# Kernel optimization log

Hardware: AMD Instinct MI355X
Metric: run time of the kernel (lower is better)

The kernel has to match this reference:

```python
import jax, jax.numpy as jnp
import numpy as np

HEADS = 8
DIM_HEAD = 64
SCALE = DIM_HEAD ** -0.5
LN_EPS = 1e-5


def setup_inputs() -> dict:
    key = jax.random.key(0)
    ks = jax.random.split(key, 4)
    b, n, dim = 8, 1024, 512
    inner = HEADS * DIM_HEAD  # 512
    return {
        "x": jax.random.normal(ks[0], (b, n, dim), dtype=jnp.float32),
        "w_qkv": jax.random.normal(ks[1], (dim, 3 * inner), dtype=jnp.float32) * (dim ** -0.5),
        "reattn_w": jax.random.normal(ks[2], (HEADS, HEADS), dtype=jnp.float32),
        "ln_g": jnp.ones((HEADS,), dtype=jnp.float32),
        "ln_b": jnp.zeros((HEADS,), dtype=jnp.float32),
        "w_out": jax.random.normal(ks[3], (inner, dim), dtype=jnp.float32) * (inner ** -0.5),
        "b_out": jnp.zeros((dim,), dtype=jnp.float32),
    }


def reference(x, w_qkv, reattn_w, ln_g, ln_b, w_out, b_out):
    b, n, dim = x.shape
    h, d = HEADS, DIM_HEAD
    qkv = x @ w_qkv  # [b, n, 3*h*d]
    q, k, v = jnp.split(qkv, 3, axis=-1)
    to_heads = lambda t: t.reshape(b, n, h, d).transpose(0, 2, 1, 3)  # [b,h,n,d]
    q, k, v = to_heads(q), to_heads(k), to_heads(v)

    dots = jnp.einsum('bhid,bhjd->bhij', q, k) * SCALE
    attn = jax.nn.softmax(dots, axis=-1)  # dropout = 0 -> identity

    # cross-head re-mixing: b h i j, h g -> b g i j
    attn = jnp.einsum('bhij,hg->bgij', attn, reattn_w)

    # LayerNorm over the head dimension (axis=1 of [b,h,i,j])
    mu = jnp.mean(attn, axis=1, keepdims=True)
    var = jnp.var(attn, axis=1, keepdims=True)
    reattn = (attn - mu) * jax.lax.rsqrt(var + LN_EPS)
    reattn = reattn * ln_g[None, :, None, None] + ln_b[None, :, None, None]

    out = jnp.einsum('bhij,bhjd->bhid', reattn, v)
    out = out.transpose(0, 2, 1, 3).reshape(b, n, h * d)  # [b, n, inner]
    return out @ w_out + b_out
```

## Files before the change

kernel.cpp:

```cpp
#include <hip/hip_runtime.h>
#include <hip/hip_bf16.h>

typedef short bf16x8 __attribute__((ext_vector_type(8)));
typedef float f32x4 __attribute__((ext_vector_type(4)));

__device__ inline unsigned short f2bf(float f) {
    union { float f; unsigned u; } c; c.f = f;
    unsigned r = c.u + 0x7fffu + ((c.u >> 16) & 1u);
    return (unsigned short)(r >> 16);
}
__device__ inline float bf2f(unsigned short u) {
    union { unsigned u; float f; } c; c.u = ((unsigned)u) << 16; return c.f;
}
__device__ inline unsigned cvt_pk_bf16(float lo, float hi) {
    unsigned r;
    asm("v_cvt_pk_bf16_f32 %0, %1, %2" : "=v"(r) : "v"(lo), "v"(hi));
    return r;
}
__device__ inline float fast_exp2(float x) {
#if __has_builtin(__builtin_amdgcn_exp2f)
    return __builtin_amdgcn_exp2f(x);
#else
    return __exp2f(x);
#endif
}

__global__ __launch_bounds__(256) void k_f32_to_bf16(const float* __restrict__ in,
                                                     unsigned short* __restrict__ out, int n4) {
    int i = blockIdx.x * 256 + threadIdx.x;
    if (i >= n4) return;
    f32x4 v = *(const f32x4*)&in[(size_t)i * 4];
    ushort4 o;
    o.x = f2bf(v[0]); o.y = f2bf(v[1]); o.z = f2bf(v[2]); o.w = f2bf(v[3]);
    *(ushort4*)&out[(size_t)i * 4] = o;
}

__global__ __launch_bounds__(256) void k_transpose_bf16(const float* __restrict__ in,
                                                        unsigned short* __restrict__ out,
                                                        int K, int N) {
    int idx = blockIdx.x * 256 + threadIdx.x;
    if (idx >= N * K) return;
    int n = idx / K, k = idx % K;
    out[idx] = f2bf(in[(size_t)k * N + n]);
}

__global__ __launch_bounds__(256) void k_relayout(const unsigned short* __restrict__ qkv,
                                                  unsigned short* __restrict__ kt2,
                                                  unsigned short* __restrict__ vt2) {
    const int bh = blockIdx.y;
    const int b = bh >> 3, h = bh & 7;
    const int jt = blockIdx.x;
    const int t = threadIdx.x;
    __shared__ unsigned short tile[32][72];
    const int j = t >> 3, dc = (t & 7) * 8;
    const size_t qbase = (size_t)(b * 1024 + jt * 32 + j) * 1536;
    const size_t chunk = ((size_t)bh * 32 + jt) * 2048;
    bf16x8 kv = *(const bf16x8*)&qkv[qbase + 512 + h * 64 + dc];
    *(bf16x8*)&kt2[chunk + (dc >> 5) * 1024 + j * 32 + (dc & 31)] = kv;
    bf16x8 vv = *(const bf16x8*)&qkv[qbase + 1024 + h * 64 + dc];
    *(bf16x8*)&tile[j][dc] = vv;
    __syncthreads();
    const int d = t >> 2, j0 = (t & 3) * 8;
    union { bf16x8 v; unsigned short s[8]; } pk;
#pragma unroll
    for (int e = 0; e < 8; ++e) pk.s[e] = tile[j0 + e][d];
    *(bf16x8*)&vt2[chunk + d * 32 + j0] = pk.v;
}

template <int BM, int BN, int BK, bool OUT_BF16, bool HAS_BIAS>
__global__ __launch_bounds__(256) void gemm_bt(
    const unsigned short* __restrict__ A, int ldA, long long sA,
    const unsigned short* __restrict__ B, int ldB, long long sB,
    void* __restrict__ Cv, int ldC, long long sC,
    const float* __restrict__ bias, float scale, int K) {
    constexpr int PAD = 8, LDR = BK + PAD;
    __shared__ __align__(16) unsigned short As[BM * LDR];
    __shared__ __align__(16) unsigned short Bs[BN * LDR];

    const int tid = threadIdx.x;
    const int lane = tid & 63, wv = tid >> 6;
    const int wm = wv >> 1, wn = wv & 1;
    constexpr int WM = BM / 2, WN = BN / 2;
    constexpr int MF = WM / 16, NF = WN / 16;
    constexpr int KG = BK / 8;

    const int m0 = blockIdx.x * BM, n0 = blockIdx.y * BN;
    A += (long long)blockIdx.z * sA;
    B += (long long)blockIdx.z * sB;

    const int lr = lane & 15, lk = (lane >> 4) * 8;

    f32x4 acc[MF][NF];
#pragma unroll
    for (int m = 0; m < MF; ++m)
#pragma unroll
        for (int n = 0; n < NF; ++n) acc[m][n] = (f32x4){0.f, 0.f, 0.f, 0.f};

    for (int k0 = 0; k0 < K; k0 += BK) {
#pragma unroll
        for (int i = 0; i < BM * KG / 256; ++i) {
            int c = i * 256 + tid;
            int row = c / KG, kg = c % KG;
            *(bf16x8*)&As[row * LDR + kg * 8] =
                *(const bf16x8*)&A[(size_t)(m0 + row) * ldA + k0 + kg * 8];
        }
#pragma unroll
        for (int i = 0; i < BN * KG / 256; ++i) {
            int c = i * 256 + tid;
            int row = c / KG, kg = c % KG;
            *(bf16x8*)&Bs[row * LDR + kg * 8] =
                *(const bf16x8*)&B[(size_t)(n0 + row) * ldB + k0 + kg * 8];
        }
        __syncthreads();
#pragma unroll
        for (int kk = 0; kk < BK; kk += 32) {
            bf16x8 af[MF], bfr[NF];
#pragma unroll
            for (int m = 0; m < MF; ++m)
                af[m] = *(const bf16x8*)&As[(wm * WM + m * 16 + lr) * LDR + kk + lk];
#pragma unroll
            for (int n = 0; n < NF; ++n)
                bfr[n] = *(const bf16x8*)&Bs[(wn * WN + n * 16 + lr) * LDR + kk + lk];
#pragma unroll
            for (int m = 0; m < MF; ++m)
#pragma unroll
                for (int n = 0; n < NF; ++n)
                    acc[m][n] = __builtin_amdgcn_mfma_f32_16x16x32_bf16(af[m], bfr[n], acc[m][n], 0, 0, 0);
        }
        __syncthreads();
    }

    const int rb = (lane >> 4) * 4;
    const long long cbase = (long long)blockIdx.z * sC;
#pragma unroll
    for (int m = 0; m < MF; ++m) {
#pragma unroll
        for (int n = 0; n < NF; ++n) {
            int col = n0 + wn * WN + n * 16 + lr;
            float bv = HAS_BIAS ? bias[col] : 0.0f;
#pragma unroll
            for (int r = 0; r < 4; ++r) {
                int row = m0 + wm * WM + m * 16 + rb + r;
                float v = acc[m][n][r] * scale + bv;
                if constexpr (OUT_BF16)
                    ((unsigned short*)Cv)[cbase + (size_t)row * ldC + col] = f2bf(v);
                else
                    ((float*)Cv)[cbase + (size_t)row * ldC + col] = v;
            }
        }
    }
}

#define C_SCALE 0.18033688f

__global__ __launch_bounds__(512) void attn_fused(
    const unsigned short* __restrict__ qkv,
    const unsigned short* __restrict__ kt2,
    const unsigned short* __restrict__ vt2,
    unsigned short* __restrict__ pvout,
    const float* __restrict__ Wm,
    const float* __restrict__ ln_g, const float* __restrict__ ln_b) {
    const int blk = blockIdx.x;
    const int b = blk & 7, it = blk >> 3;
    const int i0 = it * 32;
    const int tid = threadIdx.x;
    const int lane = tid & 63, h = tid >> 6;
    const int lr = lane & 15, qq = lane >> 4;

    __shared__ __align__(16) unsigned short Ps[32 * 32 * 8];
    __shared__ __align__(16) unsigned short Rs[8 * 32 * 40];
    __shared__ __align__(16) unsigned short Wa[16 * 8];
    __shared__ __align__(16) unsigned short zst[8];

    if (tid < 128) {
        int g = tid >> 3, hh = tid & 7;
        float v = 0.f;
        if (g < 8) {
            float s = 0.f;
#pragma unroll
            for (int g2 = 0; g2 < 8; ++g2) s += Wm[hh * 8 + g2];
            v = Wm[hh * 8 + g] - s * 0.125f;
        }
        Wa[g * 8 + hh] = f2bf(v);
    }
    if (tid < 8) zst[tid] = 0;

    const int hi4 = qq & 1;
    float gm[4], bt[4];
#pragma unroll
    for (int r = 0; r < 4; ++r) {
        gm[r] = ln_g[hi4 * 4 + r];
        bt[r] = ln_b[hi4 * 4 + r];
    }

    bf16x8 qf[2][2];
#pragma unroll
    for (int ni = 0; ni < 2; ++ni)
#pragma unroll
        for (int kk = 0; kk < 2; ++kk) {
            bf16x8 raw = *(const bf16x8*)&qkv[(size_t)(b * 1024 + i0 + ni * 16 + lr) * 1536 +
                                              h * 64 + kk * 32 + qq * 8];
            union { bf16x8 v; unsigned u[4]; } pk;
#pragma unroll
            for (int e = 0; e < 4; ++e)
                pk.u[e] = cvt_pk_bf16(bf2f((unsigned short)raw[2 * e]) * C_SCALE,
                                      bf2f((unsigned short)raw[2 * e + 1]) * C_SCALE);
            qf[ni][kk] = pk.v;
        }

    const unsigned short* kbase = kt2 + ((size_t)(b * 8 + h)) * 32 * 2048;
    const unsigned short* vbase = vt2 + ((size_t)(b * 8 + h)) * 32 * 2048;
    const int kfo0 = lr * 32 + qq * 8;
    const int kfo1 = (16 + lr) * 32 + qq * 8;

    float lacc[2] = {0.f, 0.f};
    bf16x8 kC0 = *(const bf16x8*)(kbase + kfo0);
    bf16x8 kC1 = *(const bf16x8*)(kbase + 1024 + kfo0);
    bf16x8 kC2 = *(const bf16x8*)(kbase + kfo1);
    bf16x8 kC3 = *(const bf16x8*)(kbase + 1024 + kfo1);
    for (int n = 0; n < 32; ++n) {
        int np = (n + 1) & 31;
        const unsigned short* kch = kbase + (size_t)np * 2048;
        bf16x8 kN0 = *(const bf16x8*)(kch + kfo0);
        bf16x8 kN1 = *(const bf16x8*)(kch + 1024 + kfo0);
        bf16x8 kN2 = *(const bf16x8*)(kch + kfo1);
        bf16x8 kN3 = *(const bf16x8*)(kch + 1024 + kfo1);
        f32x4 a[2][2];
#pragma unroll
        for (int mf = 0; mf < 2; ++mf)
#pragma unroll
            for (int ni = 0; ni < 2; ++ni) a[mf][ni] = (f32x4){0.f, 0.f, 0.f, 0.f};
#pragma unroll
        for (int ni = 0; ni < 2; ++ni) {
            a[0][ni] = __builtin_amdgcn_mfma_f32_16x16x32_bf16(kC0, qf[ni][0], a[0][ni], 0, 0, 0);
            a[0][ni] = __builtin_amdgcn_mfma_f32_16x16x32_bf16(kC1, qf[ni][1], a[0][ni], 0, 0, 0);
            a[1][ni] = __builtin_amdgcn_mfma_f32_16x16x32_bf16(kC2, qf[ni][0], a[1][ni], 0, 0, 0);
            a[1][ni] = __builtin_amdgcn_mfma_f32_16x16x32_bf16(kC3, qf[ni][1], a[1][ni], 0, 0, 0);
        }
#pragma unroll
        for (int ni = 0; ni < 2; ++ni)
#pragma unroll
            for (int mf = 0; mf < 2; ++mf)
#pragma unroll
                for (int rr = 0; rr < 4; ++rr) lacc[ni] += fast_exp2(a[mf][ni][rr]);
        kC0 = kN0; kC1 = kN1; kC2 = kN2; kC3 = kN3;
    }
#pragma unroll
    for (int ni = 0; ni < 2; ++ni) {
        lacc[ni] += __shfl_xor(lacc[ni], 16);
        lacc[ni] += __shfl_xor(lacc[ni], 32);
    }
    float llog[2] = { __log2f(lacc[0]), __log2f(lacc[1]) };

    __syncthreads();

    bf16x8 wfrag = *(const bf16x8*)((qq == 0) ? (const void*)&Wa[lr * 8] : (const void*)zst);

    f32x4 o[2][4];
#pragma unroll
    for (int pp = 0; pp < 2; ++pp)
#pragma unroll
        for (int nd = 0; nd < 4; ++nd) o[pp][nd] = (f32x4){0.f, 0.f, 0.f, 0.f};

    const int vfo = lr * 32 + qq * 8;

    for (int n = 0; n < 32; ++n) {
        const unsigned short* vch = vbase + (size_t)n * 2048;
        bf16x8 vf[4];
#pragma unroll
        for (int nd = 0; nd < 4; ++nd)
            vf[nd] = *(const bf16x8*)(vch + nd * 512 + vfo);
        int np = (n + 1) & 31;
        const unsigned short* kch = kbase + (size_t)np * 2048;
        bf16x8 kN0 = *(const bf16x8*)(kch + kfo0);
        bf16x8 kN1 = *(const bf16x8*)(kch + 1024 + kfo0);
        bf16x8 kN2 = *(const bf16x8*)(kch + kfo1);
        bf16x8 kN3 = *(const bf16x8*)(kch + 1024 + kfo1);

        f32x4 a[2][2];
#pragma unroll
        for (int mf = 0; mf < 2; ++mf)
#pragma unroll
            for (int ni = 0; ni < 2; ++ni) a[mf][ni] = (f32x4){0.f, 0.f, 0.f, 0.f};
#pragma unroll
        for (int ni = 0; ni < 2; ++ni) {
            a[0][ni] = __builtin_amdgcn_mfma_f32_16x16x32_bf16(kC0, qf[ni][0], a[0][ni], 0, 0, 0);
            a[0][ni] = __builtin_amdgcn_mfma_f32_16x16x32_bf16(kC1, qf[ni][1], a[0][ni], 0, 0, 0);
            a[1][ni] = __builtin_amdgcn_mfma_f32_16x16x32_bf16(kC2, qf[ni][0], a[1][ni], 0, 0, 0);
            a[1][ni] = __builtin_amdgcn_mfma_f32_16x16x32_bf16(kC3, qf[ni][1], a[1][ni], 0, 0, 0);
        }

#pragma unroll
        for (int ni = 0; ni < 2; ++ni) {
            const int i = ni * 16 + lr;
            const int ibase = i * 32;
#pragma unroll
            for (int mf = 0; mf < 2; ++mf) {
                const int jb = mf * 16 + qq * 4;
#pragma unroll
                for (int rr = 0; rr < 4; ++rr) {
                    float p = fast_exp2(a[mf][ni][rr] - llog[ni]);
                    int jr = (jb + rr + 5 * i) & 31;
                    Ps[(ibase + jr) * 8 + h] = f2bf(p);
                }
            }
        }
        __syncthreads();

#pragma unroll
        for (int z = 0; z < 8; ++z) {
            const int ii = h * 4 + (z & 3), jh = z >> 2;
            const int jcol = jh * 16 + lr;
            const void* paddr = (qq == 0)
                ? (const void*)&Ps[(ii * 32 + ((jcol + 5 * ii) & 31)) * 8]
                : (const void*)zst;
            bf16x8 pf = *(const bf16x8*)paddr;
            f32x4 d = __builtin_amdgcn_mfma_f32_16x16x32_bf16(wfrag, pf,
                        (f32x4){0.f, 0.f, 0.f, 0.f}, 0, 0, 0);
            float s2 = d[0] * d[0] + d[1] * d[1];
            s2 = fmaf(d[2], d[2], s2);
            s2 = fmaf(d[3], d[3], s2);
            s2 += __shfl_xor(s2, 16);
            float rs = rsqrtf(s2 * 0.125f + 1e-5f);
            if (lane < 32) {
                const int gb = hi4 * 4;
#pragma unroll
                for (int r = 0; r < 4; ++r)
                    Rs[((gb + r) * 32 + ii) * 40 + jcol] =
                        f2bf(d[r] * rs * gm[r] + bt[r]);
            }
        }
        __syncthreads();

#pragma unroll
        for (int pp = 0; pp < 2; ++pp) {
            bf16x8 rf = *(const bf16x8*)&Rs[(h * 32 + pp * 16 + lr) * 40 + qq * 8];
#pragma unroll
            for (int nd = 0; nd < 4; ++nd)
                o[pp][nd] = __builtin_amdgcn_mfma_f32_16x16x32_bf16(rf, vf[nd], o[pp][nd], 0, 0, 0);
        }
        kC0 = kN0; kC1 = kN1; kC2 = kN2; kC3 = kN3;
    }

#pragma unroll
    for (int pp = 0; pp < 2; ++pp)
#pragma unroll
        for (int nd = 0; nd < 4; ++nd)
#pragma unroll
            for (int rr = 0; rr < 4; ++rr) {
                int i = i0 + pp * 16 + qq * 4 + rr;
                int d = nd * 16 + lr;
                pvout[(size_t)(b * 1024 + i) * 512 + h * 64 + d] = f2bf(o[pp][nd][rr]);
            }
}

extern "C" void kernel_launch(void* const* d_in, const int* in_sizes, int n_in,
                              void* d_out, int out_size, void* d_ws, size_t ws_size,
                              hipStream_t stream) {
    const float* x        = (const float*)d_in[0];
    const float* w_qkv    = (const float*)d_in[1];
    const float* reattn_w = (const float*)d_in[2];
    const float* ln_g     = (const float*)d_in[3];
    const float* ln_b     = (const float*)d_in[4];
    const float* w_out    = (const float*)d_in[5];
    const float* b_out    = (const float*)d_in[6];
    float* out = (float*)d_out;

    char* ws = (char*)d_ws;
    unsigned short* x_bf  = (unsigned short*)(ws + 0);
    unsigned short* wqkvT = (unsigned short*)(ws + 8388608);
    unsigned short* woutT = (unsigned short*)(ws + 9961472);
    unsigned short* qkv   = (unsigned short*)(ws + 10485760);
    unsigned short* kt2   = (unsigned short*)(ws + 35651584);
    unsigned short* vt2   = (unsigned short*)(ws + 44040192);
    unsigned short* pv    = (unsigned short*)(ws + 52428800);

    k_f32_to_bf16<<<4096, 256, 0, stream>>>(x, x_bf, 1048576);
    k_transpose_bf16<<<3072, 256, 0, stream>>>(w_qkv, wqkvT, 512, 1536);
    k_transpose_bf16<<<1024, 256, 0, stream>>>(w_out, woutT, 512, 512);

    gemm_bt<128, 128, 64, true, false><<<dim3(64, 12, 1), 256, 0, stream>>>(
        x_bf, 512, 0, wqkvT, 512, 0, qkv, 1536, 0, nullptr, 1.0f, 512);

    k_relayout<<<dim3(32, 64), 256, 0, stream>>>(qkv, kt2, vt2);

    attn_fused<<<256, 512, 0, stream>>>(qkv, kt2, vt2, pv, reattn_w, ln_g, ln_b);

    gemm_bt<128, 128, 64, false, true><<<dim3(64, 4, 1), 256, 0, stream>>>(
        pv, 512, 0, woutT, 512, 0, out, 512, 0, b_out, 1.0f, 512);
}
```

Baseline: 155.1 us.

## Halve attention query tile to 16 rows and double grid size

The fused attention kernel now processes 16 query rows per block instead of 32, launching 512 blocks, with a min-blocks launch bound of 4 to cap register use. The softmax normalisation is folded into the MFMA accumulator init (negative log-sum), and bf16 conversions are packed pairwise. The aim is better occupancy and CU coverage on a 256-CU part at the cost of reloading K and V twice as often per query row.

```diff
diff --git a/kernel.cpp b/kernel.cpp
--- a/kernel.cpp
+++ b/kernel.cpp
@@ -153,7 +153,7 @@
 
 #define C_SCALE 0.18033688f
 
-__global__ __launch_bounds__(512) void attn_fused(
+__global__ __launch_bounds__(512, 4) void attn_fused(
     const unsigned short* __restrict__ qkv,
     const unsigned short* __restrict__ kt2,
     const unsigned short* __restrict__ vt2,
@@ -162,13 +162,13 @@
     const float* __restrict__ ln_g, const float* __restrict__ ln_b) {
     const int blk = blockIdx.x;
     const int b = blk & 7, it = blk >> 3;
-    const int i0 = it * 32;
+    const int i0 = it * 16;
     const int tid = threadIdx.x;
     const int lane = tid & 63, h = tid >> 6;
     const int lr = lane & 15, qq = lane >> 4;
 
-    __shared__ __align__(16) unsigned short Ps[32 * 32 * 8];
-    __shared__ __align__(16) unsigned short Rs[8 * 32 * 40];
+    __shared__ __align__(16) unsigned short Ps[16 * 32 * 8];
+    __shared__ __align__(16) unsigned short Rs[8 * 16 * 40];
     __shared__ __align__(16) unsigned short Wa[16 * 8];
     __shared__ __align__(16) unsigned short zst[8];
 
@@ -193,27 +193,25 @@
         bt[r] = ln_b[hi4 * 4 + r];
     }
 
-    bf16x8 qf[2][2];
-#pragma unroll
-    for (int ni = 0; ni < 2; ++ni)
-#pragma unroll
-        for (int kk = 0; kk < 2; ++kk) {
-            bf16x8 raw = *(const bf16x8*)&qkv[(size_t)(b * 1024 + i0 + ni * 16 + lr) * 1536 +
-                                              h * 64 + kk * 32 + qq * 8];
-            union { bf16x8 v; unsigned u[4]; } pk;
-#pragma unroll
-            for (int e = 0; e < 4; ++e)
-                pk.u[e] = cvt_pk_bf16(bf2f((unsigned short)raw[2 * e]) * C_SCALE,
-                                      bf2f((unsigned short)raw[2 * e + 1]) * C_SCALE);
-            qf[ni][kk] = pk.v;
-        }
+    bf16x8 qf[2];
+#pragma unroll
+    for (int kk = 0; kk < 2; ++kk) {
+        bf16x8 raw = *(const bf16x8*)&qkv[(size_t)(b * 1024 + i0 + lr) * 1536 +
+                                          h * 64 + kk * 32 + qq * 8];
+        union { bf16x8 v; unsigned u[4]; } pk;
+#pragma unroll
+        for (int e = 0; e < 4; ++e)
+            pk.u[e] = cvt_pk_bf16(bf2f((unsigned short)raw[2 * e]) * C_SCALE,
+                                  bf2f((unsigned short)raw[2 * e + 1]) * C_SCALE);
+        qf[kk] = pk.v;
+    }
 
     const unsigned short* kbase = kt2 + ((size_t)(b * 8 + h)) * 32 * 2048;
     const unsigned short* vbase = vt2 + ((size_t)(b * 8 + h)) * 32 * 2048;
     const int kfo0 = lr * 32 + qq * 8;
     const int kfo1 = (16 + lr) * 32 + qq * 8;
 
-    float lacc[2] = {0.f, 0.f};
+    float lacc = 0.f;
     bf16x8 kC0 = *(const bf16x8*)(kbase + kfo0);
     bf16x8 kC1 = *(const bf16x8*)(kbase + 1024 + kfo0);
     bf16x8 kC2 = *(const bf16x8*)(kbase + kfo1);
@@ -225,44 +223,29 @@
         bf16x8 kN1 = *(const bf16x8*)(kch + 1024 + kfo0);
         bf16x8 kN2 = *(const bf16x8*)(kch + kfo1);
         bf16x8 kN3 = *(const bf16x8*)(kch + 1024 + kfo1);
-        f32x4 a[2][2];
-#pragma unroll
-        for (int mf = 0; mf < 2; ++mf)
-#pragma unroll
-            for (int ni = 0; ni < 2; ++ni) a[mf][ni] = (f32x4){0.f, 0.f, 0.f, 0.f};
-#pragma unroll
-        for (int ni = 0; ni < 2; ++ni) {
-            a[0][ni] = __builtin_amdgcn_mfma_f32_16x16x32_bf16(kC0, qf[ni][0], a[0][ni], 0, 0, 0);
-            a[0][ni] = __builtin_amdgcn_mfma_f32_16x16x32_bf16(kC1, qf[ni][1], a[0][ni], 0, 0, 0);
-            a[1][ni] = __builtin_amdgcn_mfma_f32_16x16x32_bf16(kC2, qf[ni][0], a[1][ni], 0, 0, 0);
-            a[1][ni] = __builtin_amdgcn_mfma_f32_16x16x32_bf16(kC3, qf[ni][1], a[1][ni], 0, 0, 0);
-        }
-#pragma unroll
-        for (int ni = 0; ni < 2; ++ni)
-#pragma unroll
-            for (int mf = 0; mf < 2; ++mf)
-#pragma unroll
-                for (int rr = 0; rr < 4; ++rr) lacc[ni] += fast_exp2(a[mf][ni][rr]);
+        f32x4 a0 = (f32x4){0.f, 0.f, 0.f, 0.f}, a1 = (f32x4){0.f, 0.f, 0.f, 0.f};
+        a0 = __builtin_amdgcn_mfma_f32_16x16x32_bf16(kC0, qf[0], a0, 0, 0, 0);
+        a0 = __builtin_amdgcn_mfma_f32_16x16x32_bf16(kC1, qf[1], a0, 0, 0, 0);
+        a1 = __builtin_amdgcn_mfma_f32_16x16x32_bf16(kC2, qf[0], a1, 0, 0, 0);
+        a1 = __builtin_amdgcn_mfma_f32_16x16x32_bf16(kC3, qf[1], a1, 0, 0, 0);
+#pragma unroll
+        for (int rr = 0; rr < 4; ++rr) lacc += fast_exp2(a0[rr]) + fast_exp2(a1[rr]);
         kC0 = kN0; kC1 = kN1; kC2 = kN2; kC3 = kN3;
     }
-#pragma unroll
-    for (int ni = 0; ni < 2; ++ni) {
-        lacc[ni] += __shfl_xor(lacc[ni], 16);
-        lacc[ni] += __shfl_xor(lacc[ni], 32);
-    }
-    float llog[2] = { __log2f(lacc[0]), __log2f(lacc[1]) };
+    lacc += __shfl_xor(lacc, 16);
+    lacc += __shfl_xor(lacc, 32);
+    const float nllog = -__log2f(lacc);
 
     __syncthreads();
 
     bf16x8 wfrag = *(const bf16x8*)((qq == 0) ? (const void*)&Wa[lr * 8] : (const void*)zst);
 
-    f32x4 o[2][4];
-#pragma unroll
-    for (int pp = 0; pp < 2; ++pp)
-#pragma unroll
-        for (int nd = 0; nd < 4; ++nd) o[pp][nd] = (f32x4){0.f, 0.f, 0.f, 0.f};
+    f32x4 o[4];
+#pragma unroll
+    for (int nd = 0; nd < 4; ++nd) o[nd] = (f32x4){0.f, 0.f, 0.f, 0.f};
 
     const int vfo = lr * 32 + qq * 8;
+    const f32x4 cinit = (f32x4){nllog, nllog, nllog, nllog};
 
     for (int n = 0; n < 32; ++n) {
         const unsigned short* vch = vbase + (size_t)n * 2048;
@@ -277,39 +260,30 @@
         bf16x8 kN2 = *(const bf16x8*)(kch + kfo1);
         bf16x8 kN3 = *(const bf16x8*)(kch + 1024 + kfo1);
 
-        f32x4 a[2][2];
-#pragma unroll
-        for (int mf = 0; mf < 2; ++mf)
-#pragma unroll
-            for (int ni = 0; ni < 2; ++ni) a[mf][ni] = (f32x4){0.f, 0.f, 0.f, 0.f};
-#pragma unroll
-        for (int ni = 0; ni < 2; ++ni) {
-            a[0][ni] = __builtin_amdgcn_mfma_f32_16x16x32_bf16(kC0, qf[ni][0], a[0][ni], 0, 0, 0);
-            a[0][ni] = __builtin_amdgcn_mfma_f32_16x16x32_bf16(kC1, qf[ni][1], a[0][ni], 0, 0, 0);
-            a[1][ni] = __builtin_amdgcn_mfma_f32_16x16x32_bf16(kC2, qf[ni][0], a[1][ni], 0, 0, 0);
-            a[1][ni] = __builtin_amdgcn_mfma_f32_16x16x32_bf16(kC3, qf[ni][1], a[1][ni], 0, 0, 0);
-        }
-
-#pragma unroll
-        for (int ni = 0; ni < 2; ++ni) {
-            const int i = ni * 16 + lr;
-            const int ibase = i * 32;
-#pragma unroll
-            for (int mf = 0; mf < 2; ++mf) {
-                const int jb = mf * 16 + qq * 4;
-#pragma unroll
-                for (int rr = 0; rr < 4; ++rr) {
-                    float p = fast_exp2(a[mf][ni][rr] - llog[ni]);
-                    int jr = (jb + rr + 5 * i) & 31;
-                    Ps[(ibase + jr) * 8 + h] = f2bf(p);
-                }
-            }
+        f32x4 a0 = cinit, a1 = cinit;
+        a0 = __builtin_amdgcn_mfma_f32_16x16x32_bf16(kC0, qf[0], a0, 0, 0, 0);
+        a0 = __builtin_amdgcn_mfma_f32_16x16x32_bf16(kC1, qf[1], a0, 0, 0, 0);
+        a1 = __builtin_amdgcn_mfma_f32_16x16x32_bf16(kC2, qf[0], a1, 0, 0, 0);
+        a1 = __builtin_amdgcn_mfma_f32_16x16x32_bf16(kC3, qf[1], a1, 0, 0, 0);
+
+#pragma unroll
+        for (int mf = 0; mf < 2; ++mf) {
+            f32x4 a = mf ? a1 : a0;
+            unsigned u01 = cvt_pk_bf16(fast_exp2(a[0]), fast_exp2(a[1]));
+            unsigned u23 = cvt_pk_bf16(fast_exp2(a[2]), fast_exp2(a[3]));
+            const int jb = mf * 16 + qq * 4;
+            const int ibase = lr * 32;
+            const int rot = 5 * lr;
+            Ps[(ibase + ((jb + 0 + rot) & 31)) * 8 + h] = (unsigned short)u01;
+            Ps[(ibase + ((jb + 1 + rot) & 31)) * 8 + h] = (unsigned short)(u01 >> 16);
+            Ps[(ibase + ((jb + 2 + rot) & 31)) * 8 + h] = (unsigned short)u23;
+            Ps[(ibase + ((jb + 3 + rot) & 31)) * 8 + h] = (unsigned short)(u23 >> 16);
         }
         __syncthreads();
 
 #pragma unroll
-        for (int z = 0; z < 8; ++z) {
-            const int ii = h * 4 + (z & 3), jh = z >> 2;
+        for (int z = 0; z < 4; ++z) {
+            const int ii = h * 2 + (z >> 1), jh = z & 1;
             const int jcol = jh * 16 + lr;
             const void* paddr = (qq == 0)
                 ? (const void*)&Ps[(ii * 32 + ((jcol + 5 * ii) & 31)) * 8]
@@ -324,34 +298,33 @@
             float rs = rsqrtf(s2 * 0.125f + 1e-5f);
             if (lane < 32) {
                 const int gb = hi4 * 4;
-#pragma unroll
-                for (int r = 0; r < 4; ++r)
-                    Rs[((gb + r) * 32 + ii) * 40 + jcol] =
-                        f2bf(d[r] * rs * gm[r] + bt[r]);
+                unsigned pk0 = cvt_pk_bf16(d[0] * rs * gm[0] + bt[0], d[1] * rs * gm[1] + bt[1]);
+                unsigned pk1 = cvt_pk_bf16(d[2] * rs * gm[2] + bt[2], d[3] * rs * gm[3] + bt[3]);
+                Rs[((gb + 0) * 16 + ii) * 40 + jcol] = (unsigned short)pk0;
+                Rs[((gb + 1) * 16 + ii) * 40 + jcol] = (unsigned short)(pk0 >> 16);
+                Rs[((gb + 2) * 16 + ii) * 40 + jcol] = (unsigned short)pk1;
+                Rs[((gb + 3) * 16 + ii) * 40 + jcol] = (unsigned short)(pk1 >> 16);
             }
         }
         __syncthreads();
 
-#pragma unroll
-        for (int pp = 0; pp < 2; ++pp) {
-            bf16x8 rf = *(const bf16x8*)&Rs[(h * 32 + pp * 16 + lr) * 40 + qq * 8];
+        {
+            bf16x8 rf = *(const bf16x8*)&Rs[(h * 16 + lr) * 40 + qq * 8];
 #pragma unroll
             for (int nd = 0; nd < 4; ++nd)
-                o[pp][nd] = __builtin_amdgcn_mfma_f32_16x16x32_bf16(rf, vf[nd], o[pp][nd], 0, 0, 0);
+                o[nd] = __builtin_amdgcn_mfma_f32_16x16x32_bf16(rf, vf[nd], o[nd], 0, 0, 0);
         }
         kC0 = kN0; kC1 = kN1; kC2 = kN2; kC3 = kN3;
     }
 
 #pragma unroll
-    for (int pp = 0; pp < 2; ++pp)
-#pragma unroll
-        for (int nd = 0; nd < 4; ++nd)
-#pragma unroll
-            for (int rr = 0; rr < 4; ++rr) {
-                int i = i0 + pp * 16 + qq * 4 + rr;
-                int d = nd * 16 + lr;
-                pvout[(size_t)(b * 1024 + i) * 512 + h * 64 + d] = f2bf(o[pp][nd][rr]);
-            }
+    for (int nd = 0; nd < 4; ++nd)
+#pragma unroll
+        for (int rr = 0; rr < 4; ++rr) {
+            int i = i0 + qq * 4 + rr;
+            int d = nd * 16 + lr;
+            pvout[(size_t)(b * 1024 + i) * 512 + h * 64 + d] = f2bf(o[nd][rr]);
+        }
 }
 
 extern "C" void kernel_launch(void* const* d_in, const int* in_sizes, int n_in,
@@ -384,7 +357,7 @@
 
     k_relayout<<<dim3(32, 64), 256, 0, stream>>>(qkv, kt2, vt2);
 
-    attn_fused<<<256, 512, 0, stream>>>(qkv, kt2, vt2, pv, reattn_w, ln_g, ln_b);
+    attn_fused<<<512, 512, 0, stream>>>(qkv, kt2, vt2, pv, reattn_w, ln_g, ln_b);
 
     gemm_bt<128, 128, 64, false, true><<<dim3(64, 4, 1), 256, 0, stream>>>(
         pv, 512, 0, woutT, 512, 0, out, 512, 0, b_out, 1.0f, 512);
```

After: 158.7 us. 2.3% more time.

## Split softmax normalizer pass into a separate high-parallelism kernel

Applied to the files above, without the earlier changes.

Moves the first pass (computing per-row log-sum-exp of QK^T) out of the fused attention kernel into its own kernel with 1024 blocks of 256 threads, one wave per 16 query rows per head. That kernel writes the negated log2 normalizer to workspace. The fused kernel reads it and uses it as the MFMA accumulator initial value, which removes the per-element subtraction before exp2. The aim is to run the compute-heavy normalizer pass across many more blocks than the 256-block fused kernel can. In exchange it adds a kernel launch, a small global round trip, and recomputes Q fragments and K loads in both kernels.

```diff
diff --git a/kernel.cpp b/kernel.cpp
--- a/kernel.cpp
+++ b/kernel.cpp
@@ -153,67 +153,36 @@
 
 #define C_SCALE 0.18033688f
 
-__global__ __launch_bounds__(512) void attn_fused(
+__global__ __launch_bounds__(256) void k_pass1(
     const unsigned short* __restrict__ qkv,
     const unsigned short* __restrict__ kt2,
-    const unsigned short* __restrict__ vt2,
-    unsigned short* __restrict__ pvout,
-    const float* __restrict__ Wm,
-    const float* __restrict__ ln_g, const float* __restrict__ ln_b) {
+    float* __restrict__ nllog) {
     const int blk = blockIdx.x;
-    const int b = blk & 7, it = blk >> 3;
-    const int i0 = it * 32;
+    const int b = blk & 7, r = blk >> 3;
+    const int h = r & 7, it = r >> 3;
     const int tid = threadIdx.x;
-    const int lane = tid & 63, h = tid >> 6;
+    const int lane = tid & 63, w = tid >> 6;
     const int lr = lane & 15, qq = lane >> 4;
-
-    __shared__ __align__(16) unsigned short Ps[32 * 32 * 8];
-    __shared__ __align__(16) unsigned short Rs[8 * 32 * 40];
-    __shared__ __align__(16) unsigned short Wa[16 * 8];
-    __shared__ __align__(16) unsigned short zst[8];
-
-    if (tid < 128) {
-        int g = tid >> 3, hh = tid & 7;
-        float v = 0.f;
-        if (g < 8) {
-            float s = 0.f;
-#pragma unroll
-            for (int g2 = 0; g2 < 8; ++g2) s += Wm[hh * 8 + g2];
-            v = Wm[hh * 8 + g] - s * 0.125f;
-        }
-        Wa[g * 8 + hh] = f2bf(v);
-    }
-    if (tid < 8) zst[tid] = 0;
-
-    const int hi4 = qq & 1;
-    float gm[4], bt[4];
-#pragma unroll
-    for (int r = 0; r < 4; ++r) {
-        gm[r] = ln_g[hi4 * 4 + r];
-        bt[r] = ln_b[hi4 * 4 + r];
-    }
-
-    bf16x8 qf[2][2];
-#pragma unroll
-    for (int ni = 0; ni < 2; ++ni)
-#pragma unroll
-        for (int kk = 0; kk < 2; ++kk) {
-            bf16x8 raw = *(const bf16x8*)&qkv[(size_t)(b * 1024 + i0 + ni * 16 + lr) * 1536 +
-                                              h * 64 + kk * 32 + qq * 8];
-            union { bf16x8 v; unsigned u[4]; } pk;
-#pragma unroll
-            for (int e = 0; e < 4; ++e)
-                pk.u[e] = cvt_pk_bf16(bf2f((unsigned short)raw[2 * e]) * C_SCALE,
-                                      bf2f((unsigned short)raw[2 * e + 1]) * C_SCALE);
-            qf[ni][kk] = pk.v;
-        }
+    const int i0 = it * 64 + w * 16;
+
+    bf16x8 qf[2];
+#pragma unroll
+    for (int kk = 0; kk < 2; ++kk) {
+        bf16x8 raw = *(const bf16x8*)&qkv[(size_t)(b * 1024 + i0 + lr) * 1536 +
+                                          h * 64 + kk * 32 + qq * 8];
+        union { bf16x8 v; unsigned u[4]; } pk;
+#pragma unroll
+        for (int e = 0; e < 4; ++e)
+            pk.u[e] = cvt_pk_bf16(bf2f((unsigned short)raw[2 * e]) * C_SCALE,
+                                  bf2f((unsigned short)raw[2 * e + 1]) * C_SCALE);
+        qf[kk] = pk.v;
+    }
 
     const unsigned short* kbase = kt2 + ((size_t)(b * 8 + h)) * 32 * 2048;
-    const unsigned short* vbase = vt2 + ((size_t)(b * 8 + h)) * 32 * 2048;
     const int kfo0 = lr * 32 + qq * 8;
-    const int kfo1 = (16 + lr) * 32 + qq * 8;
-
-    float lacc[2] = {0.f, 0.f};
+    const int kfo1 = kfo0 + 512;
+
+    float lacc = 0.f;
     bf16x8 kC0 = *(const bf16x8*)(kbase + kfo0);
     bf16x8 kC1 = *(const bf16x8*)(kbase + 1024 + kfo0);
     bf16x8 kC2 = *(const bf16x8*)(kbase + kfo1);
@@ -225,32 +194,88 @@
         bf16x8 kN1 = *(const bf16x8*)(kch + 1024 + kfo0);
         bf16x8 kN2 = *(const bf16x8*)(kch + kfo1);
         bf16x8 kN3 = *(const bf16x8*)(kch + 1024 + kfo1);
-        f32x4 a[2][2];
-#pragma unroll
-        for (int mf = 0; mf < 2; ++mf)
-#pragma unroll
-            for (int ni = 0; ni < 2; ++ni) a[mf][ni] = (f32x4){0.f, 0.f, 0.f, 0.f};
-#pragma unroll
-        for (int ni = 0; ni < 2; ++ni) {
-            a[0][ni] = __builtin_amdgcn_mfma_f32_16x16x32_bf16(kC0, qf[ni][0], a[0][ni], 0, 0, 0);
-            a[0][ni] = __builtin_amdgcn_mfma_f32_16x16x32_bf16(kC1, qf[ni][1], a[0][ni], 0, 0, 0);
-            a[1][ni] = __builtin_amdgcn_mfma_f32_16x16x32_bf16(kC2, qf[ni][0], a[1][ni], 0, 0, 0);
-            a[1][ni] = __builtin_amdgcn_mfma_f32_16x16x32_bf16(kC3, qf[ni][1], a[1][ni], 0, 0, 0);
-        }
-#pragma unroll
-        for (int ni = 0; ni < 2; ++ni)
-#pragma unroll
-            for (int mf = 0; mf < 2; ++mf)
-#pragma unroll
-                for (int rr = 0; rr < 4; ++rr) lacc[ni] += fast_exp2(a[mf][ni][rr]);
+        f32x4 a0 = (f32x4){0.f, 0.f, 0.f, 0.f}, a1 = (f32x4){0.f, 0.f, 0.f, 0.f};
+        a0 = __builtin_amdgcn_mfma_f32_16x16x32_bf16(kC0, qf[0], a0, 0, 0, 0);
+        a0 = __builtin_amdgcn_mfma_f32_16x16x32_bf16(kC1, qf[1], a0, 0, 0, 0);
+        a1 = __builtin_amdgcn_mfma_f32_16x16x32_bf16(kC2, qf[0], a1, 0, 0, 0);
+        a1 = __builtin_amdgcn_mfma_f32_16x16x32_bf16(kC3, qf[1], a1, 0, 0, 0);
+#pragma unroll
+        for (int rr = 0; rr < 4; ++rr) lacc += fast_exp2(a0[rr]) + fast_exp2(a1[rr]);
         kC0 = kN0; kC1 = kN1; kC2 = kN2; kC3 = kN3;
     }
+    lacc += __shfl_xor(lacc, 16);
+    lacc += __shfl_xor(lacc, 32);
+    if (qq == 0) nllog[((b * 8 + h) << 10) + i0 + lr] = -__log2f(lacc);
+}
+
+__global__ __launch_bounds__(512) void attn_fused(
+    const unsigned short* __restrict__ qkv,
+    const unsigned short* __restrict__ kt2,
+    const unsigned short* __restrict__ vt2,
+    const float* __restrict__ nllog,
+    unsigned short* __restrict__ pvout,
+    const float* __restrict__ Wm,
+    const float* __restrict__ ln_g, const float* __restrict__ ln_b) {
+    const int blk = blockIdx.x;
+    const int b = blk & 7, it = blk >> 3;
+    const int i0 = it * 32;
+    const int tid = threadIdx.x;
+    const int lane = tid & 63, h = tid >> 6;
+    const int lr = lane & 15, qq = lane >> 4;
+
+    __shared__ __align__(16) unsigned short Ps[32 * 32 * 8];
+    __shared__ __align__(16) unsigned short Rs[8 * 32 * 40];
+    __shared__ __align__(16) unsigned short Wa[16 * 8];
+    __shared__ __align__(16) unsigned short zst[8];
+
+    if (tid < 128) {
+        int g = tid >> 3, hh = tid & 7;
+        float v = 0.f;
+        if (g < 8) {
+            float s = 0.f;
+#pragma unroll
+            for (int g2 = 0; g2 < 8; ++g2) s += Wm[hh * 8 + g2];
+            v = Wm[hh * 8 + g] - s * 0.125f;
+        }
+        Wa[g * 8 + hh] = f2bf(v);
+    }
+    if (tid < 8) zst[tid] = 0;
+
+    const int hi4 = qq & 1;
+    float gm[4], bt[4];
+#pragma unroll
+    for (int r = 0; r < 4; ++r) {
+        gm[r] = ln_g[hi4 * 4 + r];
+        bt[r] = ln_b[hi4 * 4 + r];
+    }
+
+    bf16x8 qf[2][2];
+#pragma unroll
+    for (int ni = 0; ni < 2; ++ni)
+#pragma unroll
+        for (int kk = 0; kk < 2; ++kk) {
+            bf16x8 raw = *(const bf16x8*)&qkv[(size_t)(b * 1024 + i0 + ni * 16 + lr) * 1536 +
+                                              h * 64 + kk * 32 + qq * 8];
+            union { bf16x8 v; unsigned u[4]; } pk;
+#pragma unroll
+            for (int e = 0; e < 4; ++e)
+                pk.u[e] = cvt_pk_bf16(bf2f((unsigned short)raw[2 * e]) * C_SCALE,
+                                      bf2f((unsigned short)raw[2 * e + 1]) * C_SCALE);
+            qf[ni][kk] = pk.v;
+        }
+
+    f32x4 cinit[2];
 #pragma unroll
     for (int ni = 0; ni < 2; ++ni) {
-        lacc[ni] += __shfl_xor(lacc[ni], 16);
-        lacc[ni] += __shfl_xor(lacc[ni], 32);
-    }
-    float llog[2] = { __log2f(lacc[0]), __log2f(lacc[1]) };
+        float v = nllog[((b * 8 + h) << 10) + i0 + ni * 16 + lr];
+        cinit[ni] = (f32x4){v, v, v, v};
+    }
+
+    const unsigned short* kbase = kt2 + ((size_t)(b * 8 + h)) * 32 * 2048;
+    const unsigned short* vbase = vt2 + ((size_t)(b * 8 + h)) * 32 * 2048;
+    const int kfo0 = lr * 32 + qq * 8;
+    const int kfo1 = (16 + lr) * 32 + qq * 8;
+    const int vfo = lr * 32 + qq * 8;
 
     __syncthreads();
 
@@ -262,7 +287,10 @@
 #pragma unroll
         for (int nd = 0; nd < 4; ++nd) o[pp][nd] = (f32x4){0.f, 0.f, 0.f, 0.f};
 
-    const int vfo = lr * 32 + qq * 8;
+    bf16x8 kC0 = *(const bf16x8*)(kbase + kfo0);
+    bf16x8 kC1 = *(const bf16x8*)(kbase + 1024 + kfo0);
+    bf16x8 kC2 = *(const bf16x8*)(kbase + kfo1);
+    bf16x8 kC3 = *(const bf16x8*)(kbase + 1024 + kfo1);
 
     for (int n = 0; n < 32; ++n) {
         const unsigned short* vch = vbase + (size_t)n * 2048;
@@ -279,9 +307,7 @@
 
         f32x4 a[2][2];
 #pragma unroll
-        for (int mf = 0; mf < 2; ++mf)
-#pragma unroll
-            for (int ni = 0; ni < 2; ++ni) a[mf][ni] = (f32x4){0.f, 0.f, 0.f, 0.f};
+        for (int ni = 0; ni < 2; ++ni) { a[0][ni] = cinit[ni]; a[1][ni] = cinit[ni]; }
 #pragma unroll
         for (int ni = 0; ni < 2; ++ni) {
             a[0][ni] = __builtin_amdgcn_mfma_f32_16x16x32_bf16(kC0, qf[ni][0], a[0][ni], 0, 0, 0);
@@ -299,7 +325,7 @@
                 const int jb = mf * 16 + qq * 4;
 #pragma unroll
                 for (int rr = 0; rr < 4; ++rr) {
-                    float p = fast_exp2(a[mf][ni][rr] - llog[ni]);
+                    float p = fast_exp2(a[mf][ni][rr]);
                     int jr = (jb + rr + 5 * i) & 31;
                     Ps[(ibase + jr) * 8 + h] = f2bf(p);
                 }
@@ -309,8 +335,8 @@
 
 #pragma unroll
         for (int z = 0; z < 8; ++z) {
-            const int ii = h * 4 + (z & 3), jh = z >> 2;
-            const int jcol = jh * 16 + lr;
+            const int ii = h * 4 + (z & 3), jz = z >> 2;
+            const int jcol = jz * 16 + lr;
             const void* paddr = (qq == 0)
                 ? (const void*)&Ps[(ii * 32 + ((jcol + 5 * ii) & 31)) * 8]
                 : (const void*)zst;
@@ -374,6 +400,7 @@
     unsigned short* kt2   = (unsigned short*)(ws + 35651584);
     unsigned short* vt2   = (unsigned short*)(ws + 44040192);
     unsigned short* pv    = (unsigned short*)(ws + 52428800);
+    float*          nllog = (float*)(ws + 60817408);
 
     k_f32_to_bf16<<<4096, 256, 0, stream>>>(x, x_bf, 1048576);
     k_transpose_bf16<<<3072, 256, 0, stream>>>(w_qkv, wqkvT, 512, 1536);
@@ -384,7 +411,9 @@
 
     k_relayout<<<dim3(32, 64), 256, 0, stream>>>(qkv, kt2, vt2);
 
-    attn_fused<<<256, 512, 0, stream>>>(qkv, kt2, vt2, pv, reattn_w, ln_g, ln_b);
+    k_pass1<<<1024, 256, 0, stream>>>(qkv, kt2, nllog);
+
+    attn_fused<<<256, 512, 0, stream>>>(qkv, kt2, vt2, nllog, pv, reattn_w, ln_g, ln_b);
 
     gemm_bt<128, 128, 64, false, true><<<dim3(64, 4, 1), 256, 0, stream>>>(
         pv, 512, 0, woutT, 512, 0, out, 512, 0, b_out, 1.0f, 512);
```

After: 171.9 us. +10.8%, slower.
